# Optimization experiments

Measured on AMD Instinct MI355X. Metric: run time of the kernel, lower is better.

The kernel has to match this reference:

```python
import jax, jax.numpy as jnp
import numpy as np

B, S, D, H = 8, 1024, 768, 12
DH = D // H  # 64

def setup_inputs() -> dict:
    key = jax.random.key(0)
    ks = jax.random.split(key, 8)
    return {
        "hidden_states": jax.random.normal(ks[0], (B, S, D), jnp.float32),
        "attention_mask": jnp.zeros((B, 1, 1, S), jnp.float32),
        "click_times": jax.random.uniform(ks[1], (B, S), jnp.float32),
        "Wq": jax.random.normal(ks[2], (D, D), jnp.float32) * 0.02,
        "bq": jnp.zeros((D,), jnp.float32),
        "Wk": jax.random.normal(ks[3], (D, D), jnp.float32) * 0.02,
        "bk": jnp.zeros((D,), jnp.float32),
        "Wv": jax.random.normal(ks[4], (D, D), jnp.float32) * 0.02,
        "bv": jnp.zeros((D,), jnp.float32),
    }

def reference(hidden_states, attention_mask, click_times, Wq, bq, Wk, bk, Wv, bv):
    # Linear projections (torch Linear: x @ W.T + b)
    q = hidden_states @ Wq.T + bq
    k = hidden_states @ Wk.T + bk
    v = hidden_states @ Wv.T + bv
    # [B,S,D] -> [B,H,S,DH]
    def split_heads(x):
        return x.reshape(B, S, H, DH).transpose(0, 2, 1, 3)
    q, k, v = split_heads(q), split_heads(k), split_heads(v)
    scores = jnp.einsum('bhqd,bhkd->bhqk', q, k) / jnp.sqrt(jnp.float32(DH))
    # click_times gate: [B,S] -> [B,1,1,S], multiplicative on scores
    scores = scores * click_times[:, None, None, :]
    scores = scores + attention_mask
    probs = jax.nn.softmax(scores, axis=-1)  # dropout is identity at eval
    ctx = jnp.einsum('bhqk,bhkd->bhqd', probs, v)
    ctx = ctx.transpose(0, 2, 1, 3).reshape(B, S, D)
    return ctx
```

## Files before the change

kernel.cpp:

```cpp
#include <hip/hip_runtime.h>
#include <hip/hip_bf16.h>

#define BB 8
#define SS 1024
#define DD 768
#define HH 12
#define LOG2E 1.4426950408889634f

typedef __attribute__((ext_vector_type(8))) _Float16 f16x8;
typedef __attribute__((ext_vector_type(4))) _Float16 f16x4;
typedef __attribute__((ext_vector_type(4))) float f32x4;

typedef __attribute__((address_space(3))) void lds_void;
typedef const __attribute__((address_space(1))) void gmem_void;
#define GLOAD_LDS16(src, dst) \
    __builtin_amdgcn_global_load_lds((gmem_void*)(src), (lds_void*)(dst), 16, 0, 0)

__global__ void prep_kernel(const float* __restrict__ X,
                            const float* __restrict__ Wq,
                            const float* __restrict__ Wk,
                            const float* __restrict__ Wv,
                            const float* __restrict__ bq,
                            const float* __restrict__ bk,
                            const float* __restrict__ bv,
                            const float* __restrict__ click,
                            const float* __restrict__ mask,
                            _Float16* __restrict__ Xh,
                            _Float16* __restrict__ Wh,
                            float* __restrict__ bias,
                            float* __restrict__ ckS,
                            float* __restrict__ mkL) {
    const int NX4 = (BB * SS * DD) / 4;
    const int NW4 = (DD * DD) / 4;
    const int tid = blockIdx.x * blockDim.x + threadIdx.x;
    const int nth = gridDim.x * blockDim.x;

    for (int i = tid; i < NX4; i += nth) {
        f32x4 x = ((const f32x4*)X)[i];
        f16x4 h;
        for (int j = 0; j < 4; ++j) h[j] = (_Float16)x[j];
        ((f16x4*)Xh)[i] = h;
    }
    for (int i = tid; i < 3 * NW4; i += nth) {
        const float* src = (i < NW4) ? Wq : (i < 2 * NW4 ? Wk : Wv);
        const int ii = (i < NW4) ? i : (i < 2 * NW4 ? i - NW4 : i - 2 * NW4);
        f32x4 x = ((const f32x4*)src)[ii];
        f16x4 h;
        for (int j = 0; j < 4; ++j) h[j] = (_Float16)x[j];
        ((f16x4*)Wh)[i] = h;
    }
    for (int i = tid; i < 3 * DD; i += nth) {
        bias[i] = (i < DD) ? bq[i] : (i < 2 * DD ? bk[i - DD] : bv[i - 2 * DD]);
    }
    for (int i = tid; i < BB * SS; i += nth) {
        ckS[i] = (0.125f * LOG2E) * click[i];
        mkL[i] = LOG2E * mask[i];
    }
}

__global__ __launch_bounds__(256, 3) void qkv_gemm(const _Float16* __restrict__ Xh,
                                                   const _Float16* __restrict__ Wh,
                                                   const float* __restrict__ bias,
                                                   _Float16* __restrict__ Qb,
                                                   _Float16* __restrict__ Kb,
                                                   _Float16* __restrict__ Vt) {
    __shared__ __align__(16) _Float16 At[2][128 * 32];
    __shared__ __align__(16) _Float16 Bt[2][192 * 32];

    const int tid = threadIdx.x;
    const int l = tid & 63, w = tid >> 6;
    const int wm = w >> 1, wn = w & 1;

    const int bid = blockIdx.x;
    const int nid = (bid & 7) * 96 + (bid >> 3);
    const int bx = nid / 12;
    const int by = nid - bx * 12;
    const int mblk = bx * 128, nblk = by * 192;

    const int lr = l & 15, lg = l >> 4;
    const int mbase = mblk + wm * 64, nbase = nblk + wn * 96;

    const int sr_i = l >> 2;
    const int scb  = (l & 3) << 4;
    const int sx   = (sr_i >> 1) & 3;
    const int scol = (scb ^ (sx << 4)) >> 1;

    const _Float16* Ag = Xh + (size_t)(mblk + w * 32 + sr_i) * DD + scol;
    const _Float16* Bg = Wh + (size_t)(nblk + w * 48 + sr_i) * DD + scol;

    const int ax = (lr >> 1) & 3;
    const int acol = (lg ^ ax) << 3;
    const int arow0 = (wm * 64 + lr) * 32 + acol;
    const int brow0 = (wn * 96 + lr) * 32 + acol;

    f32x4 acc[4][6] = {};

#pragma unroll
    for (int i = 0; i < 2; ++i)
        GLOAD_LDS16(Ag + i * 16 * DD, &At[0][w * 1024 + i * 512]);
#pragma unroll
    for (int i = 0; i < 3; ++i)
        GLOAD_LDS16(Bg + i * 16 * DD, &Bt[0][w * 1536 + i * 512]);
    __syncthreads();

    for (int s_ = 0; s_ < 24; ++s_) {
        const int cur = s_ & 1;
        if (s_ < 23) {
            const int kk = (s_ + 1) * 32;
#pragma unroll
            for (int i = 0; i < 2; ++i)
                GLOAD_LDS16(Ag + kk + i * 16 * DD, &At[cur ^ 1][w * 1024 + i * 512]);
#pragma unroll
            for (int i = 0; i < 3; ++i)
                GLOAD_LDS16(Bg + kk + i * 16 * DD, &Bt[cur ^ 1][w * 1536 + i * 512]);
        }
        f16x8 a[4];
#pragma unroll
        for (int mi = 0; mi < 4; ++mi)
            a[mi] = *(const f16x8*)(&At[cur][arow0 + mi * 512]);
        __builtin_amdgcn_s_setprio(1);
#pragma unroll
        for (int ni = 0; ni < 6; ++ni) {
            const f16x8 b = *(const f16x8*)(&Bt[cur][brow0 + ni * 512]);
#pragma unroll
            for (int mi = 0; mi < 4; ++mi)
                acc[mi][ni] = __builtin_amdgcn_mfma_f32_16x16x32_f16(
                    a[mi], b, acc[mi][ni], 0, 0, 0);
        }
        __builtin_amdgcn_s_setprio(0);
        __syncthreads();
    }

#pragma unroll
    for (int ni = 0; ni < 6; ++ni) {
        const int n = nbase + ni * 16 + lr;
        const float bv_ = bias[n];
        const int proj = (n >= 2 * DD) ? 2 : (n >= DD ? 1 : 0);
        const int rem = n - proj * DD;
        const int h = rem >> 6, dh = rem & 63;
#pragma unroll
        for (int mi = 0; mi < 4; ++mi) {
            const int m0 = mbase + mi * 16 + lg * 4;
            const int b_ = m0 >> 10;
            const int s0 = m0 & 1023;
            const int bh = b_ * HH + h;
            f32x4 v = acc[mi][ni];
            if (proj == 2) {
                f16x4 pk;
#pragma unroll
                for (int r = 0; r < 4; ++r) pk[r] = (_Float16)(v[r] + bv_);
                *(f16x4*)(Vt + ((size_t)bh * 64 + dh) * SS + s0) = pk;
            } else {
                _Float16* dst = (proj == 0) ? Qb : Kb;
#pragma unroll
                for (int r = 0; r < 4; ++r)
                    dst[((size_t)bh * SS + (s0 + r)) * 64 + dh] =
                        (_Float16)(v[r] + bv_);
            }
        }
    }
}

__global__ __launch_bounds__(256, 3) void attn_kernel(const _Float16* __restrict__ Qb,
                                                      const _Float16* __restrict__ Kb,
                                                      const _Float16* __restrict__ Vt,
                                                      const float* __restrict__ ckS,
                                                      const float* __restrict__ mkL,
                                                      float* __restrict__ out) {
    __shared__ __align__(16) _Float16 Ksh[2][64 * 64];
    __shared__ __align__(16) _Float16 Vsh[2][64 * 64];
    __shared__ __align__(16) _Float16 pT[4][2][16][40];

    const int tid = threadIdx.x;
    const int l = tid & 63, w = tid >> 6;
    const int lr = l & 15, lg = l >> 4;

    const int bid = blockIdx.x;
    const int nid = (bid & 7) * 96 + (bid >> 3);
    const int qt2 = nid & 7;
    const int bh  = nid >> 3;
    const int b_ = bh / HH, h = bh - b_ * HH;
    const int qb0 = qt2 * 128 + w * 16;

    const _Float16* Qp = Qb + (size_t)bh * (SS * 64);
    const _Float16* Kp = Kb + (size_t)bh * (SS * 64);
    const _Float16* Vp = Vt + (size_t)bh * (SS * 64);
    const float* ck = ckS + b_ * SS;
    const float* mk = mkL + b_ * SS;

    f16x8 qf[2][2];
#pragma unroll
    for (int u = 0; u < 2; ++u) {
        qf[u][0] = *(const f16x8*)(Qp + (size_t)(qb0 + u * 64 + lr) * 64 + lg * 8);
        qf[u][1] = *(const f16x8*)(Qp + (size_t)(qb0 + u * 64 + lr) * 64 + 32 + lg * 8);
    }

    const int srow = l >> 3;
    const int scb  = (l & 7) << 4;
    const int scol = (scb ^ (srow << 4)) >> 1;
    const _Float16* Kg = Kp + (size_t)(w * 16 + srow) * 64 + scol;
    const _Float16* Vg = Vp + (size_t)(w * 16 + srow) * SS + scol;

#pragma unroll
    for (int i = 0; i < 2; ++i) {
        GLOAD_LDS16(Kg + (size_t)(i * 8) * 64, &Ksh[0][w * 1024 + i * 512]);
        GLOAD_LDS16(Vg + (size_t)(i * 8) * SS, &Vsh[0][w * 1024 + i * 512]);
    }
    __syncthreads();

    f32x4 o[2][4] = {};
    float m_run[2] = {-3.0e38f, -3.0e38f};
    float l_run[2] = {0.f, 0.f};
    const int sw = (lr & 7) << 4;

    for (int c = 0; c < 16; ++c) {
        const int cur = c & 1;
        if (c < 15) {
            const int nb = (c + 1) * 64;
#pragma unroll
            for (int i = 0; i < 2; ++i) {
                GLOAD_LDS16(Kg + (size_t)(nb + i * 8) * 64, &Ksh[cur ^ 1][w * 1024 + i * 512]);
                GLOAD_LDS16(Vg + nb + (size_t)(i * 8) * SS, &Vsh[cur ^ 1][w * 1024 + i * 512]);
            }
        }
        const _Float16* Ks = Ksh[cur];
        const _Float16* Vs = Vsh[cur];
        const int cb64 = c * 64;

#pragma unroll
        for (int ks = 0; ks < 2; ++ks) {
            f32x4 st[2][2];
            __builtin_amdgcn_s_setprio(1);
#pragma unroll
            for (int t = 0; t < 2; ++t) {
                const int row = (ks * 2 + t) * 16 + lr;
                const f16x8 kf0 = *(const f16x8*)(Ks + row * 64 + (((lg << 4) ^ sw) >> 1));
                const f16x8 kf1 = *(const f16x8*)(Ks + row * 64 + (((64 | (lg << 4)) ^ sw) >> 1));
#pragma unroll
                for (int u = 0; u < 2; ++u) {
                    f32x4 z = {};
                    z = __builtin_amdgcn_mfma_f32_16x16x32_f16(kf0, qf[u][0], z, 0, 0, 0);
                    st[u][t] = __builtin_amdgcn_mfma_f32_16x16x32_f16(kf1, qf[u][1], z, 0, 0, 0);
                }
            }
            __builtin_amdgcn_s_setprio(0);

            const int koff = cb64 + ks * 32 + lg * 4;
            const f32x4 ck0 = *(const f32x4*)(ck + koff);
            const f32x4 ck1 = *(const f32x4*)(ck + koff + 16);
            const f32x4 mk0 = *(const f32x4*)(mk + koff);
            const f32x4 mk1 = *(const f32x4*)(mk + koff + 16);

#pragma unroll
            for (int u = 0; u < 2; ++u) {
                float s0[4], s1[4];
#pragma unroll
                for (int r = 0; r < 4; ++r) {
                    s0[r] = st[u][0][r] * ck0[r] + mk0[r];
                    s1[r] = st[u][1][r] * ck1[r] + mk1[r];
                }
                float tmax = fmaxf(fmaxf(fmaxf(s0[0], s0[1]), fmaxf(s0[2], s0[3])),
                                   fmaxf(fmaxf(s1[0], s1[1]), fmaxf(s1[2], s1[3])));
                tmax = fmaxf(tmax, __shfl_xor(tmax, 16));
                tmax = fmaxf(tmax, __shfl_xor(tmax, 32));

                if (__any(tmax - m_run[u] > 11.5415603f)) {
                    const float m_new = fmaxf(m_run[u], tmax);
                    const float sc = __builtin_amdgcn_exp2f(m_run[u] - m_new);
                    l_run[u] *= sc;
#pragma unroll
                    for (int f = 0; f < 4; ++f)
#pragma unroll
                        for (int r = 0; r < 4; ++r) o[u][f][r] *= sc;
                    m_run[u] = m_new;
                }

                float psum = 0.f;
                f16x4 pk0, pk1;
#pragma unroll
                for (int r = 0; r < 4; ++r) {
                    const float p0 = __builtin_amdgcn_exp2f(s0[r] - m_run[u]);
                    const float p1 = __builtin_amdgcn_exp2f(s1[r] - m_run[u]);
                    psum += p0 + p1;
                    pk0[r] = (_Float16)p0;
                    pk1[r] = (_Float16)p1;
                }
                l_run[u] += psum;

                *(f16x4*)(&pT[w][u][lr][lg * 4]) = pk0;
                *(f16x4*)(&pT[w][u][lr][16 + lg * 4]) = pk1;
            }

            const f16x8 pb0 = *(const f16x8*)(&pT[w][0][lr][lg * 8]);
            const f16x8 pb1 = *(const f16x8*)(&pT[w][1][lr][lg * 8]);

            __builtin_amdgcn_s_setprio(1);
#pragma unroll
            for (int f = 0; f < 4; ++f) {
                const int vrow = f * 16 + lr;
                const f16x8 vf = *(const f16x8*)(Vs + vrow * 64 +
                                                 ((((ks << 6) | (lg << 4)) ^ sw) >> 1));
                o[0][f] = __builtin_amdgcn_mfma_f32_16x16x32_f16(vf, pb0, o[0][f], 0, 0, 0);
                o[1][f] = __builtin_amdgcn_mfma_f32_16x16x32_f16(vf, pb1, o[1][f], 0, 0, 0);
            }
            __builtin_amdgcn_s_setprio(0);
        }
        __syncthreads();
    }

#pragma unroll
    for (int u = 0; u < 2; ++u) {
        float lt = l_run[u];
        lt += __shfl_xor(lt, 16);
        lt += __shfl_xor(lt, 32);
        const float inv = 1.f / lt;
#pragma unroll
        for (int f = 0; f < 4; ++f) {
            f32x4 v = o[u][f];
#pragma unroll
            for (int r = 0; r < 4; ++r) v[r] *= inv;
            float* dst = out + ((size_t)(b_ * SS + qb0 + u * 64 + lr)) * DD +
                         h * 64 + f * 16 + lg * 4;
            *(f32x4*)dst = v;
        }
    }
}

extern "C" void kernel_launch(void* const* d_in, const int* in_sizes, int n_in,
                              void* d_out, int out_size, void* d_ws, size_t ws_size,
                              hipStream_t stream) {
    const float* X     = (const float*)d_in[0];
    const float* mask  = (const float*)d_in[1];
    const float* click = (const float*)d_in[2];
    const float* Wq    = (const float*)d_in[3];
    const float* bq    = (const float*)d_in[4];
    const float* Wk    = (const float*)d_in[5];
    const float* bk    = (const float*)d_in[6];
    const float* Wv    = (const float*)d_in[7];
    const float* bv    = (const float*)d_in[8];
    float* out = (float*)d_out;

    char* ws = (char*)d_ws;
    _Float16* Xh  = (_Float16*)(ws);
    _Float16* Wh  = (_Float16*)(ws + 12582912);
    float*    bia = (float*)   (ws + 16121856);
    float*    ckS = (float*)   (ws + 16131072);
    float*    mkL = (float*)   (ws + 16163840);
    _Float16* Qb  = (_Float16*)(ws + 16196608);
    _Float16* Kb  = (_Float16*)(ws + 28779520);
    _Float16* Vt  = (_Float16*)(ws + 41362432);

    prep_kernel<<<2048, 256, 0, stream>>>(X, Wq, Wk, Wv, bq, bk, bv, click, mask,
                                          Xh, Wh, bia, ckS, mkL);
    qkv_gemm<<<768, 256, 0, stream>>>(Xh, Wh, bia, Qb, Kb, Vt);
    attn_kernel<<<768, 256, 0, stream>>>(Qb, Kb, Vt, ckS, mkL, out);
}
```

Measured before the change: 181.8 us.

## Split attention work across 8 wavefronts and read V directly from global memory

The attention kernel now runs 512 threads per block, with each of the 8 wavefronts handling 16 query rows instead of 4 wavefronts handling 32 rows each. The V tile is no longer staged through double-buffered LDS: each MFMA operand is loaded straight from global memory, and only K stays in LDS. The online-softmax rescale check now tests the per-lane max first and does the cross-lane shuffle reduction only when some lane exceeds the threshold. The aim is higher occupancy, less LDS use and fewer shuffles. In exchange, V reads become strided global loads that rely on cache hits, and Q-fragment reuse per K load is halved.

```diff
diff --git a/kernel.cpp b/kernel.cpp
--- a/kernel.cpp
+++ b/kernel.cpp
@@ -161,15 +161,14 @@
     }
 }
 
-__global__ __launch_bounds__(256, 3) void attn_kernel(const _Float16* __restrict__ Qb,
+__global__ __launch_bounds__(512, 6) void attn_kernel(const _Float16* __restrict__ Qb,
                                                       const _Float16* __restrict__ Kb,
                                                       const _Float16* __restrict__ Vt,
                                                       const float* __restrict__ ckS,
                                                       const float* __restrict__ mkL,
                                                       float* __restrict__ out) {
     __shared__ __align__(16) _Float16 Ksh[2][64 * 64];
-    __shared__ __align__(16) _Float16 Vsh[2][64 * 64];
-    __shared__ __align__(16) _Float16 pT[4][2][16][40];
+    __shared__ __align__(16) _Float16 pT[8][16][40];
 
     const int tid = threadIdx.x;
     const int l = tid & 63, w = tid >> 6;
@@ -180,7 +179,7 @@
     const int qt2 = nid & 7;
     const int bh  = nid >> 3;
     const int b_ = bh / HH, h = bh - b_ * HH;
-    const int qb0 = qt2 * 128 + w * 16;
+    const int qbase = qt2 * 128 + w * 16;
 
     const _Float16* Qp = Qb + (size_t)bh * (SS * 64);
     const _Float16* Kp = Kb + (size_t)bh * (SS * 64);
@@ -188,60 +187,39 @@
     const float* ck = ckS + b_ * SS;
     const float* mk = mkL + b_ * SS;
 
-    f16x8 qf[2][2];
-#pragma unroll
-    for (int u = 0; u < 2; ++u) {
-        qf[u][0] = *(const f16x8*)(Qp + (size_t)(qb0 + u * 64 + lr) * 64 + lg * 8);
-        qf[u][1] = *(const f16x8*)(Qp + (size_t)(qb0 + u * 64 + lr) * 64 + 32 + lg * 8);
-    }
+    const f16x8 qf0 = *(const f16x8*)(Qp + (size_t)(qbase + lr) * 64 + lg * 8);
+    const f16x8 qf1 = *(const f16x8*)(Qp + (size_t)(qbase + lr) * 64 + 32 + lg * 8);
 
     const int srow = l >> 3;
-    const int scb  = (l & 7) << 4;
-    const int scol = (scb ^ (srow << 4)) >> 1;
-    const _Float16* Kg = Kp + (size_t)(w * 16 + srow) * 64 + scol;
-    const _Float16* Vg = Vp + (size_t)(w * 16 + srow) * SS + scol;
-
-#pragma unroll
-    for (int i = 0; i < 2; ++i) {
-        GLOAD_LDS16(Kg + (size_t)(i * 8) * 64, &Ksh[0][w * 1024 + i * 512]);
-        GLOAD_LDS16(Vg + (size_t)(i * 8) * SS, &Vsh[0][w * 1024 + i * 512]);
-    }
+    const int scol = ((((l & 7) << 4) ^ (srow << 4)) >> 1);
+    const _Float16* Kg = Kp + (size_t)(w * 8 + srow) * 64 + scol;
+
+    GLOAD_LDS16(Kg, &Ksh[0][w * 512]);
     __syncthreads();
 
-    f32x4 o[2][4] = {};
-    float m_run[2] = {-3.0e38f, -3.0e38f};
-    float l_run[2] = {0.f, 0.f};
+    f32x4 o[4] = {};
+    float m_run = -3.0e38f, l_run = 0.f;
     const int sw = (lr & 7) << 4;
 
     for (int c = 0; c < 16; ++c) {
         const int cur = c & 1;
-        if (c < 15) {
-            const int nb = (c + 1) * 64;
-#pragma unroll
-            for (int i = 0; i < 2; ++i) {
-                GLOAD_LDS16(Kg + (size_t)(nb + i * 8) * 64, &Ksh[cur ^ 1][w * 1024 + i * 512]);
-                GLOAD_LDS16(Vg + nb + (size_t)(i * 8) * SS, &Vsh[cur ^ 1][w * 1024 + i * 512]);
-            }
-        }
+        if (c < 15)
+            GLOAD_LDS16(Kg + (size_t)(c + 1) * 64 * 64, &Ksh[cur ^ 1][w * 512]);
         const _Float16* Ks = Ksh[cur];
-        const _Float16* Vs = Vsh[cur];
         const int cb64 = c * 64;
 
 #pragma unroll
         for (int ks = 0; ks < 2; ++ks) {
-            f32x4 st[2][2];
+            f32x4 st[2];
             __builtin_amdgcn_s_setprio(1);
 #pragma unroll
             for (int t = 0; t < 2; ++t) {
                 const int row = (ks * 2 + t) * 16 + lr;
                 const f16x8 kf0 = *(const f16x8*)(Ks + row * 64 + (((lg << 4) ^ sw) >> 1));
                 const f16x8 kf1 = *(const f16x8*)(Ks + row * 64 + (((64 | (lg << 4)) ^ sw) >> 1));
-#pragma unroll
-                for (int u = 0; u < 2; ++u) {
-                    f32x4 z = {};
-                    z = __builtin_amdgcn_mfma_f32_16x16x32_f16(kf0, qf[u][0], z, 0, 0, 0);
-                    st[u][t] = __builtin_amdgcn_mfma_f32_16x16x32_f16(kf1, qf[u][1], z, 0, 0, 0);
-                }
+                f32x4 z = {};
+                z = __builtin_amdgcn_mfma_f32_16x16x32_f16(kf0, qf0, z, 0, 0, 0);
+                st[t] = __builtin_amdgcn_mfma_f32_16x16x32_f16(kf1, qf1, z, 0, 0, 0);
             }
             __builtin_amdgcn_s_setprio(0);
 
@@ -251,78 +229,70 @@
             const f32x4 mk0 = *(const f32x4*)(mk + koff);
             const f32x4 mk1 = *(const f32x4*)(mk + koff + 16);
 
-#pragma unroll
-            for (int u = 0; u < 2; ++u) {
-                float s0[4], s1[4];
-#pragma unroll
-                for (int r = 0; r < 4; ++r) {
-                    s0[r] = st[u][0][r] * ck0[r] + mk0[r];
-                    s1[r] = st[u][1][r] * ck1[r] + mk1[r];
-                }
-                float tmax = fmaxf(fmaxf(fmaxf(s0[0], s0[1]), fmaxf(s0[2], s0[3])),
-                                   fmaxf(fmaxf(s1[0], s1[1]), fmaxf(s1[2], s1[3])));
+            float s0[4], s1[4];
+#pragma unroll
+            for (int r = 0; r < 4; ++r) {
+                s0[r] = st[0][r] * ck0[r] + mk0[r];
+                s1[r] = st[1][r] * ck1[r] + mk1[r];
+            }
+            const float lmax =
+                fmaxf(fmaxf(fmaxf(s0[0], s0[1]), fmaxf(s0[2], s0[3])),
+                      fmaxf(fmaxf(s1[0], s1[1]), fmaxf(s1[2], s1[3])));
+
+            if (__any(lmax - m_run > 11.5415603f)) {
+                float tmax = lmax;
                 tmax = fmaxf(tmax, __shfl_xor(tmax, 16));
                 tmax = fmaxf(tmax, __shfl_xor(tmax, 32));
-
-                if (__any(tmax - m_run[u] > 11.5415603f)) {
-                    const float m_new = fmaxf(m_run[u], tmax);
-                    const float sc = __builtin_amdgcn_exp2f(m_run[u] - m_new);
-                    l_run[u] *= sc;
-#pragma unroll
-                    for (int f = 0; f < 4; ++f)
-#pragma unroll
-                        for (int r = 0; r < 4; ++r) o[u][f][r] *= sc;
-                    m_run[u] = m_new;
-                }
-
-                float psum = 0.f;
-                f16x4 pk0, pk1;
-#pragma unroll
-                for (int r = 0; r < 4; ++r) {
-                    const float p0 = __builtin_amdgcn_exp2f(s0[r] - m_run[u]);
-                    const float p1 = __builtin_amdgcn_exp2f(s1[r] - m_run[u]);
-                    psum += p0 + p1;
-                    pk0[r] = (_Float16)p0;
-                    pk1[r] = (_Float16)p1;
-                }
-                l_run[u] += psum;
-
-                *(f16x4*)(&pT[w][u][lr][lg * 4]) = pk0;
-                *(f16x4*)(&pT[w][u][lr][16 + lg * 4]) = pk1;
-            }
-
-            const f16x8 pb0 = *(const f16x8*)(&pT[w][0][lr][lg * 8]);
-            const f16x8 pb1 = *(const f16x8*)(&pT[w][1][lr][lg * 8]);
+                const float m_new = fmaxf(m_run, tmax);
+                const float sc = __builtin_amdgcn_exp2f(m_run - m_new);
+                l_run *= sc;
+#pragma unroll
+                for (int f = 0; f < 4; ++f)
+#pragma unroll
+                    for (int r = 0; r < 4; ++r) o[f][r] *= sc;
+                m_run = m_new;
+            }
+
+            float psum = 0.f;
+            f16x4 pk0, pk1;
+#pragma unroll
+            for (int r = 0; r < 4; ++r) {
+                const float p0 = __builtin_amdgcn_exp2f(s0[r] - m_run);
+                const float p1 = __builtin_amdgcn_exp2f(s1[r] - m_run);
+                psum += p0 + p1;
+                pk0[r] = (_Float16)p0;
+                pk1[r] = (_Float16)p1;
+            }
+            l_run += psum;
+
+            *(f16x4*)(&pT[w][lr][lg * 4]) = pk0;
+            *(f16x4*)(&pT[w][lr][16 + lg * 4]) = pk1;
+            const f16x8 pb = *(const f16x8*)(&pT[w][lr][lg * 8]);
 
             __builtin_amdgcn_s_setprio(1);
 #pragma unroll
             for (int f = 0; f < 4; ++f) {
-                const int vrow = f * 16 + lr;
-                const f16x8 vf = *(const f16x8*)(Vs + vrow * 64 +
-                                                 ((((ks << 6) | (lg << 4)) ^ sw) >> 1));
-                o[0][f] = __builtin_amdgcn_mfma_f32_16x16x32_f16(vf, pb0, o[0][f], 0, 0, 0);
-                o[1][f] = __builtin_amdgcn_mfma_f32_16x16x32_f16(vf, pb1, o[1][f], 0, 0, 0);
+                const f16x8 vf = *(const f16x8*)(Vp + (size_t)(f * 16 + lr) * SS +
+                                                 cb64 + ks * 32 + lg * 8);
+                o[f] = __builtin_amdgcn_mfma_f32_16x16x32_f16(vf, pb, o[f], 0, 0, 0);
             }
             __builtin_amdgcn_s_setprio(0);
         }
         __syncthreads();
     }
 
-#pragma unroll
-    for (int u = 0; u < 2; ++u) {
-        float lt = l_run[u];
-        lt += __shfl_xor(lt, 16);
-        lt += __shfl_xor(lt, 32);
-        const float inv = 1.f / lt;
-#pragma unroll
-        for (int f = 0; f < 4; ++f) {
-            f32x4 v = o[u][f];
-#pragma unroll
-            for (int r = 0; r < 4; ++r) v[r] *= inv;
-            float* dst = out + ((size_t)(b_ * SS + qb0 + u * 64 + lr)) * DD +
-                         h * 64 + f * 16 + lg * 4;
-            *(f32x4*)dst = v;
-        }
+    float lt = l_run;
+    lt += __shfl_xor(lt, 16);
+    lt += __shfl_xor(lt, 32);
+    const float inv = 1.f / lt;
+#pragma unroll
+    for (int f = 0; f < 4; ++f) {
+        f32x4 v = o[f];
+#pragma unroll
+        for (int r = 0; r < 4; ++r) v[r] *= inv;
+        float* dst = out + ((size_t)(b_ * SS + qbase + lr)) * DD +
+                     h * 64 + f * 16 + lg * 4;
+        *(f32x4*)dst = v;
     }
 }
 
@@ -353,5 +323,5 @@
     prep_kernel<<<2048, 256, 0, stream>>>(X, Wq, Wk, Wv, bq, bk, bv, click, mask,
                                           Xh, Wh, bia, ckS, mkL);
     qkv_gemm<<<768, 256, 0, stream>>>(Xh, Wh, bia, Qb, Kb, Vt);
-    attn_kernel<<<768, 256, 0, stream>>>(Qb, Kb, Vt, ckS, mkL, out);
+    attn_kernel<<<768, 512, 0, stream>>>(Qb, Kb, Vt, ckS, mkL, out);
 }
```

Measured after the change: 244.0 us. 1.34x slower.
